# Optimization experiments

Measured on AMD Instinct MI355X. Metric: run time of the kernel, lower is better.

## Reference

```python
import jax, jax.numpy as jnp
import numpy as np

H = 1024          # hidden_size
NH = 16           # num_attention_heads
HD = H // NH      # head_dim = 64
FF = 4096         # intermediate_size
EPS = 1e-12       # layer_norm_eps
CLAMP = 1e9


def _layer_norm(x, gamma, beta):
    mu = jnp.mean(x, axis=-1, keepdims=True)
    var = jnp.mean(jnp.square(x - mu), axis=-1, keepdims=True)
    return (x - mu) * jax.lax.rsqrt(var + EPS) * gamma + beta


def setup_inputs() -> dict:
    key = jax.random.key(0)
    ks = jax.random.split(key, 12)
    B, S = 4, 2048
    s_h = 1.0 / np.sqrt(H)
    s_f = 1.0 / np.sqrt(FF)
    return {
        "hidden_states": jax.random.normal(ks[0], (B, S, H), jnp.float32),
        "Wq": jax.random.normal(ks[1], (H, H), jnp.float32) * s_h,
        "bq": jnp.zeros((H,), jnp.float32),
        "Wk": jax.random.normal(ks[2], (H, H), jnp.float32) * s_h,
        "bk": jnp.zeros((H,), jnp.float32),
        "Wv": jax.random.normal(ks[3], (H, H), jnp.float32) * s_h,
        "bv": jnp.zeros((H,), jnp.float32),
        "ln1_g": jnp.ones((H,), jnp.float32),
        "ln1_b": jnp.zeros((H,), jnp.float32),
        "W1": jax.random.normal(ks[4], (H, FF), jnp.float32) * s_h,
        "b1": jnp.zeros((FF,), jnp.float32),
        "W2": jax.random.normal(ks[5], (FF, H), jnp.float32) * s_f,
        "b2": jnp.zeros((H,), jnp.float32),
        "ln2_g": jnp.ones((H,), jnp.float32),
        "ln2_b": jnp.zeros((H,), jnp.float32),
    }


def reference(hidden_states, Wq, bq, Wk, bk, Wv, bv, ln1_g, ln1_b,
              W1, b1, W2, b2, ln2_g, ln2_b):
    B, S, _ = hidden_states.shape
    # QKV projections -> [B, NH, S, HD]
    def heads(x):
        return x.reshape(B, S, NH, HD).transpose(0, 2, 1, 3)
    q = heads(hidden_states @ Wq + bq)
    k = heads(hidden_states @ Wk + bk)
    v = heads(hidden_states @ Wv + bv)
    # manual attention: scale, clamp, softmax + 1e-9 epsilon
    scores = jnp.einsum('bhqd,bhkd->bhqk', q, k) / np.sqrt(HD)
    scores = jnp.clip(scores, -CLAMP, CLAMP)
    probs = jax.nn.softmax(scores, axis=-1) + 1e-9
    ctx = jnp.einsum('bhqk,bhkd->bhqd', probs, v)
    ctx = ctx.transpose(0, 2, 1, 3).reshape(B, S, NH * HD)
    # residual + LN (no output projection in this module)
    x = _layer_norm(hidden_states + ctx, ln1_g, ln1_b)
    # FFN with exact gelu + clamp
    inter = jax.nn.gelu(x @ W1 + b1, approximate=False)
    inter = jnp.clip(inter, -CLAMP, CLAMP)
    out = inter @ W2 + b2
    return _layer_norm(out + x, ln2_g, ln2_b)
```

## Files before the change

kernel.cpp:

```cpp
#include <hip/hip_runtime.h>
#include <math.h>


#define H_   1024
#define NH_  16
#define HD_  64
#define FF_  4096
#define S_   2048
#define B_   4
#define BS_  (B_ * S_)

#define EPI_NONE 0
#define EPI_GELU 1
#define EPI_QKV3 2

typedef unsigned short ushort_t;
typedef short v8s __attribute__((ext_vector_type(8)));
typedef float v4f __attribute__((ext_vector_type(4)));

__device__ __forceinline__ unsigned short f2bf(float f) {
    union { float f; unsigned int u; } v; v.f = f;
    unsigned int u = v.u;
    return (unsigned short)((u + 0x7fffu + ((u >> 16) & 1u)) >> 16);
}
__device__ __forceinline__ unsigned short f2bf_rn(float f) {
    union { float f; unsigned int u; } v; v.f = f;
    return (unsigned short)((v.u + 0x8000u) >> 16);
}
__device__ __forceinline__ float bf2f(unsigned short h) {
    union { unsigned int u; float f; } v; v.u = ((unsigned int)h) << 16;
    return v.f;
}

typedef __attribute__((address_space(1))) void gvoid;
typedef __attribute__((address_space(3))) void lvoid;
__device__ __forceinline__ void async16(const void* g, void* l) {
    __builtin_amdgcn_global_load_lds((gvoid*)g, (lvoid*)l, 16, 0, 0);
}

__global__ __launch_bounds__(256)
void cast_bf16_kernel(const float* __restrict__ x, ushort_t* __restrict__ y)
{
    const size_t i = ((size_t)blockIdx.x * 256 + threadIdx.x) * 4;
    float4 v = *(const float4*)&x[i];
    ushort4 o;
    o.x = f2bf(v.x); o.y = f2bf(v.y); o.z = f2bf(v.z); o.w = f2bf(v.w);
    *(ushort4*)&y[i] = o;
}

__global__ __launch_bounds__(256)
void cast_transpose_kernel(const float* __restrict__ W, ushort_t* __restrict__ Wt,
                           int K, int N)
{
    __shared__ float tile[32][33];
    const int tid = threadIdx.x;
    const int n0 = blockIdx.x * 32, k0 = blockIdx.y * 32;
    const int r  = tid >> 3;
    const int c4 = (tid & 7) * 4;
    float4 v = *(const float4*)&W[(size_t)(k0 + r) * N + n0 + c4];
    tile[r][c4 + 0] = v.x; tile[r][c4 + 1] = v.y;
    tile[r][c4 + 2] = v.z; tile[r][c4 + 3] = v.w;
    __syncthreads();
    ushort4 o;
    o.x = f2bf(tile[c4 + 0][r]); o.y = f2bf(tile[c4 + 1][r]);
    o.z = f2bf(tile[c4 + 2][r]); o.w = f2bf(tile[c4 + 3][r]);
    *(ushort4*)&Wt[(size_t)(n0 + r) * K + k0 + c4] = o;
}

__global__ __launch_bounds__(256)
void concat3_kernel(const float* __restrict__ a, const float* __restrict__ b,
                    const float* __restrict__ c, float* __restrict__ o)
{
    const int i = blockIdx.x * 256 + threadIdx.x;
    o[i] = (i < 1024) ? a[i] : (i < 2048) ? b[i - 1024] : c[i - 2048];
}

template <int EPI>
__global__ __launch_bounds__(256)
void bgemm_kernel(const ushort_t* __restrict__ A, const ushort_t* __restrict__ Bt,
                  const float* __restrict__ bias, void* __restrict__ Cout,
                  int M, int N, int K)
{
    __shared__ ushort_t Atile[128 * 32];
    __shared__ ushort_t Btile[128 * 32];

    const int tid  = threadIdx.x;
    const int wave = tid >> 6;
    const int lane = tid & 63;
    const int ml   = lane & 15;
    const int q8   = lane >> 4;
    const int wm   = wave >> 1, wn = wave & 1;
    const int blockM = blockIdx.y * 128;
    const int blockN = blockIdx.x * 128;

    v4f acc[4][4];
#pragma unroll
    for (int a = 0; a < 4; ++a)
#pragma unroll
        for (int b = 0; b < 4; ++b) acc[a][b] = (v4f)0.f;

    for (int kt = 0; kt < K; kt += 32) {
#pragma unroll
        for (int i = 0; i < 2; ++i) {
            const int chunk = (i * 4 + wave) * 64 + lane;
            const int row = chunk >> 2;
            const int kp  = chunk & 3;
            async16(A  + (size_t)(blockM + row) * K + kt + kp * 8, &Atile[chunk * 8]);
            async16(Bt + (size_t)(blockN + row) * K + kt + kp * 8, &Btile[chunk * 8]);
        }
        __syncthreads();

        v8s af[4], bfr[4];
#pragma unroll
        for (int a = 0; a < 4; ++a)
            af[a] = *(const v8s*)&Atile[(wm * 64 + a * 16 + ml) * 32 + q8 * 8];
#pragma unroll
        for (int b = 0; b < 4; ++b)
            bfr[b] = *(const v8s*)&Btile[(wn * 64 + b * 16 + ml) * 32 + q8 * 8];
#pragma unroll
        for (int a = 0; a < 4; ++a)
#pragma unroll
            for (int b = 0; b < 4; ++b)
                acc[a][b] = __builtin_amdgcn_mfma_f32_16x16x32_bf16(
                    af[a], bfr[b], acc[a][b], 0, 0, 0);
        __syncthreads();
    }

#pragma unroll
    for (int a = 0; a < 4; ++a) {
#pragma unroll
        for (int b = 0; b < 4; ++b) {
            const int n  = blockN + wn * 64 + b * 16 + ml;
            const float bn = bias[n];
            if (EPI == EPI_QKV3) {
                const int nn = n & 1023;
                const int hh = nn >> 6, dd = nn & 63;
                ushort_t* base = (ushort_t*)Cout + (size_t)(n >> 10) * ((size_t)BS_ * H_);
                if (n < 2048) {
#pragma unroll
                    for (int r = 0; r < 4; ++r) {
                        const int m = blockM + wm * 64 + a * 16 + q8 * 4 + r;
                        base[(((size_t)((m >> 11) * NH_ + hh)) * S_ + (m & 2047)) * HD_ + dd]
                            = f2bf(acc[a][b][r] + bn);
                    }
                } else {
                    const int m0 = blockM + wm * 64 + a * 16 + q8 * 4;
                    ushort4 pk;
                    pk.x = f2bf(acc[a][b][0] + bn);
                    pk.y = f2bf(acc[a][b][1] + bn);
                    pk.z = f2bf(acc[a][b][2] + bn);
                    pk.w = f2bf(acc[a][b][3] + bn);
                    *(ushort4*)&base[(((size_t)((m0 >> 11) * NH_ + hh)) * HD_ + dd) * S_
                                     + (m0 & 2047)] = pk;
                }
            } else {
#pragma unroll
                for (int r = 0; r < 4; ++r) {
                    const int m = blockM + wm * 64 + a * 16 + q8 * 4 + r;
                    float v = acc[a][b][r] + bn;
                    if (EPI == EPI_GELU) {
                        v = v * 0.5f * (1.f + erff(v * 0.70710678118654752f));
                        v = fminf(fmaxf(v, -1e9f), 1e9f);
                        ((ushort_t*)Cout)[(size_t)m * N + n] = f2bf(v);
                    } else {
                        ((float*)Cout)[(size_t)m * N + n] = v;
                    }
                }
            }
        }
    }
}

__global__ __launch_bounds__(256)
void vsum_kernel(const ushort_t* __restrict__ VT, float* __restrict__ vsum)
{
    const int bh   = blockIdx.x;
    const int tid  = threadIdx.x;
    const int d    = tid >> 2;
    const int part = tid & 3;
    const ushort_t* p = VT + (size_t)bh * HD_ * S_ + (size_t)d * S_ + part * 512;
    float acc = 0.f;
    for (int i = 0; i < 512; i += 4) {
        ushort4 u = *(const ushort4*)&p[i];
        acc += (bf2f(u.x) + bf2f(u.y)) + (bf2f(u.z) + bf2f(u.w));
    }
    acc += __shfl_xor(acc, 1);
    acc += __shfl_xor(acc, 2);
    if (part == 0) vsum[bh * HD_ + d] = acc;
}

__global__ __launch_bounds__(256)
void flash_kernel(const ushort_t* __restrict__ Q, const ushort_t* __restrict__ Kg,
                  const ushort_t* __restrict__ VT, const float* __restrict__ vsum,
                  float* __restrict__ ctx)
{
    __shared__ ushort_t Qs[64 * 64];
    __shared__ ushort_t Ks[64 * 64];
    __shared__ ushort_t Vs[64 * 64];
    __shared__ ushort_t Pt[64 * 72];

    const int bh   = blockIdx.y;
    const int q0   = blockIdx.x * 64;
    const int tid  = threadIdx.x;
    const int wave = tid >> 6;
    const int lane = tid & 63;
    const int ml   = lane & 15;
    const int q8   = lane >> 4;
    const int sw   = ml & 7;

    const ushort_t* Qp = Q  + (size_t)bh * S_ * HD_ + (size_t)q0 * HD_;
    const ushort_t* Kp = Kg + (size_t)bh * S_ * HD_;
    const ushort_t* Vp = VT + (size_t)bh * HD_ * S_;

#pragma unroll
    for (int i = 0; i < 2; ++i) {
        const int chunk = i * 256 + tid;
        const int row = chunk >> 3, c = chunk & 7;
        async16(Qp + (size_t)row * HD_ + ((c ^ (row & 7)) * 8), &Qs[chunk * 8]);
    }

    const float C_ = 0.18033688011112042f;
    float l_r = 0.f;
    v4f o[4];
#pragma unroll
    for (int g = 0; g < 4; ++g) o[g] = (v4f)0.f;
    v8s qf0, qf1;

    const int prow = (wave * 16 + ml) * 72;

    for (int t = 0; t < S_ / 64; ++t) {
        const int kv0 = t * 64;
        __syncthreads();
#pragma unroll
        for (int i = 0; i < 2; ++i) {
            const int chunk = i * 256 + tid;
            const int row = chunk >> 3, c = chunk & 7;
            async16(Kp + (size_t)(kv0 + row) * HD_ + ((c ^ (row & 7)) * 8),
                    &Ks[chunk * 8]);
        }
#pragma unroll
        for (int i = 0; i < 2; ++i) {
            const int chunk = i * 256 + tid;
            const int row = chunk >> 3, c = chunk & 7;
            async16(Vp + (size_t)row * S_ + kv0 + ((c ^ (row & 7)) * 8),
                    &Vs[chunk * 8]);
        }
        __syncthreads();

        if (t == 0) {
            const int qrow = wave * 16 + ml;
            qf0 = *(const v8s*)&Qs[qrow * 64 + ((q8 ^ sw) * 8)];
            qf1 = *(const v8s*)&Qs[qrow * 64 + (((q8 + 4) ^ sw) * 8)];
        }

#pragma unroll
        for (int a = 0; a < 4; ++a) {
            const int krow = (a * 16 + ml) * 64;
            v8s kf0 = *(const v8s*)&Ks[krow + ((q8 ^ sw) * 8)];
            v8s kf1 = *(const v8s*)&Ks[krow + (((q8 + 4) ^ sw) * 8)];
            v4f z = (v4f)0.f;
            z = __builtin_amdgcn_mfma_f32_16x16x32_bf16(kf0, qf0, z, 0, 0, 0);
            z = __builtin_amdgcn_mfma_f32_16x16x32_bf16(kf1, qf1, z, 0, 0, 0);
            const float p0 = __builtin_exp2f(z[0] * C_);
            const float p1 = __builtin_exp2f(z[1] * C_);
            const float p2 = __builtin_exp2f(z[2] * C_);
            const float p3 = __builtin_exp2f(z[3] * C_);
            l_r += (p0 + p1) + (p2 + p3);
            ushort4 pk;
            pk.x = f2bf_rn(p0); pk.y = f2bf_rn(p1);
            pk.z = f2bf_rn(p2); pk.w = f2bf_rn(p3);
            *(ushort4*)&Pt[prow + a * 16 + q8 * 4] = pk;
        }

        v8s pf0 = *(const v8s*)&Pt[prow + q8 * 8];
        v8s pf1 = *(const v8s*)&Pt[prow + 32 + q8 * 8];
#pragma unroll
        for (int g = 0; g < 4; ++g) {
            const int vrow = (g * 16 + ml) * 64;
            v8s vf0 = *(const v8s*)&Vs[vrow + ((q8 ^ sw) * 8)];
            v8s vf1 = *(const v8s*)&Vs[vrow + (((q8 + 4) ^ sw) * 8)];
            o[g] = __builtin_amdgcn_mfma_f32_16x16x32_bf16(vf0, pf0, o[g], 0, 0, 0);
            o[g] = __builtin_amdgcn_mfma_f32_16x16x32_bf16(vf1, pf1, o[g], 0, 0, 0);
        }
    }

    l_r += __shfl_xor(l_r, 16);
    l_r += __shfl_xor(l_r, 32);

    const int bb = bh >> 4, hh = bh & 15;
    const float linv = 1.f / l_r;
    const int srow = q0 + wave * 16 + ml;
    float* cp = ctx + ((size_t)(bb * S_ + srow)) * H_ + hh * HD_;
#pragma unroll
    for (int g = 0; g < 4; ++g) {
        float4 vs4 = *(const float4*)&vsum[bh * HD_ + g * 16 + q8 * 4];
        float4 ov;
        ov.x = o[g][0] * linv + 1e-9f * vs4.x;
        ov.y = o[g][1] * linv + 1e-9f * vs4.y;
        ov.z = o[g][2] * linv + 1e-9f * vs4.z;
        ov.w = o[g][3] * linv + 1e-9f * vs4.w;
        *(float4*)&cp[g * 16 + q8 * 4] = ov;
    }
}

template <bool WB>
__global__ __launch_bounds__(256)
void add_ln_kernel(const float* __restrict__ A, const float* __restrict__ Bv,
                   const float* __restrict__ gamma, const float* __restrict__ beta,
                   float* __restrict__ out, ushort_t* __restrict__ outb)
{
    const int row = blockIdx.x;
    const int tid = threadIdx.x;
    const float* a = A  + (size_t)row * H_;
    const float* b = Bv + (size_t)row * H_;

    float4 av = *(const float4*)&a[tid * 4];
    float4 bv = *(const float4*)&b[tid * 4];
    float x[4] = { av.x + bv.x, av.y + bv.y, av.z + bv.z, av.w + bv.w };

    float s  = x[0] + x[1] + x[2] + x[3];
    float s2 = x[0]*x[0] + x[1]*x[1] + x[2]*x[2] + x[3]*x[3];
#pragma unroll
    for (int off = 1; off < 64; off <<= 1) {
        s  += __shfl_xor(s,  off);
        s2 += __shfl_xor(s2, off);
    }
    __shared__ float rs[8];
    const int wave = tid >> 6, lane = tid & 63;
    if (lane == 0) { rs[wave] = s; rs[4 + wave] = s2; }
    __syncthreads();
    const float sum  = rs[0] + rs[1] + rs[2] + rs[3];
    const float sum2 = rs[4] + rs[5] + rs[6] + rs[7];
    const float mu   = sum * (1.f / H_);
    const float var  = sum2 * (1.f / H_) - mu * mu;
    const float rstd = rsqrtf(var + 1e-12f);

    float4 gv = *(const float4*)&gamma[tid * 4];
    float4 be = *(const float4*)&beta[tid * 4];
    float4 ov;
    ov.x = (x[0] - mu) * rstd * gv.x + be.x;
    ov.y = (x[1] - mu) * rstd * gv.y + be.y;
    ov.z = (x[2] - mu) * rstd * gv.z + be.z;
    ov.w = (x[3] - mu) * rstd * gv.w + be.w;
    *(float4*)&out[(size_t)row * H_ + tid * 4] = ov;
    if (WB) {
        ushort4 ob;
        ob.x = f2bf(ov.x); ob.y = f2bf(ov.y); ob.z = f2bf(ov.z); ob.w = f2bf(ov.w);
        *(ushort4*)&outb[(size_t)row * H_ + tid * 4] = ob;
    }
}

extern "C" void kernel_launch(void* const* d_in, const int* in_sizes, int n_in,
                              void* d_out, int out_size, void* d_ws, size_t ws_size,
                              hipStream_t stream)
{
    const float* hidden = (const float*)d_in[0];
    const float* Wq     = (const float*)d_in[1];
    const float* bq     = (const float*)d_in[2];
    const float* Wk     = (const float*)d_in[3];
    const float* bk     = (const float*)d_in[4];
    const float* Wv     = (const float*)d_in[5];
    const float* bv     = (const float*)d_in[6];
    const float* ln1_g  = (const float*)d_in[7];
    const float* ln1_b  = (const float*)d_in[8];
    const float* W1     = (const float*)d_in[9];
    const float* b1     = (const float*)d_in[10];
    const float* W2     = (const float*)d_in[11];
    const float* b2     = (const float*)d_in[12];
    const float* ln2_g  = (const float*)d_in[13];
    const float* ln2_b  = (const float*)d_in[14];

    char* ws = (char*)d_ws;
    const size_t MB = 1024 * 1024;
    ushort_t* Xb    = (ushort_t*)(ws + 0);
    ushort_t* x1b   = (ushort_t*)(ws + 0);
    ushort_t* Wqt   = (ushort_t*)(ws + 16 * MB);
    ushort_t* Wkt   = (ushort_t*)(ws + 18 * MB);
    ushort_t* Wvt   = (ushort_t*)(ws + 20 * MB);
    ushort_t* W1t   = (ushort_t*)(ws + 16 * MB);
    ushort_t* W2t   = (ushort_t*)(ws + 24 * MB);
    ushort_t* q     = (ushort_t*)(ws + 32 * MB);
    ushort_t* k     = (ushort_t*)(ws + 48 * MB);
    ushort_t* vt    = (ushort_t*)(ws + 64 * MB);
    float*    ctx   = (float*)(ws + 80 * MB);
    ushort_t* inter = (ushort_t*)(ws + 32 * MB);
    float*    bcat  = (float*)(ws + 96 * MB);
    float*    vsum  = (float*)(ws + 96 * MB + 16384);
    float*    out2  = (float*)(ws + 96 * MB);
    float*    x1    = (float*)(ws + 128 * MB);
    float*    out   = (float*)d_out;

    const dim3 blk(256);

    cast_bf16_kernel<<<dim3(BS_ * H_ / 1024), blk, 0, stream>>>(hidden, Xb);
    cast_transpose_kernel<<<dim3(32, 32),  blk, 0, stream>>>(Wq, Wqt, H_, H_);
    cast_transpose_kernel<<<dim3(32, 32),  blk, 0, stream>>>(Wk, Wkt, H_, H_);
    cast_transpose_kernel<<<dim3(32, 32),  blk, 0, stream>>>(Wv, Wvt, H_, H_);
    cast_transpose_kernel<<<dim3(32, 128), blk, 0, stream>>>(W2, W2t, FF_, H_);
    concat3_kernel<<<dim3(12), blk, 0, stream>>>(bq, bk, bv, bcat);

    bgemm_kernel<EPI_QKV3><<<dim3(24, 64), blk, 0, stream>>>(
        Xb, Wqt, bcat, q, BS_, 3 * H_, H_);

    cast_transpose_kernel<<<dim3(128, 32), blk, 0, stream>>>(W1, W1t, H_, FF_);

    vsum_kernel<<<dim3(B_ * NH_), blk, 0, stream>>>(vt, vsum);

    flash_kernel<<<dim3(S_ / 64, B_ * NH_), blk, 0, stream>>>(q, k, vt, vsum, ctx);

    add_ln_kernel<true><<<dim3(BS_), blk, 0, stream>>>(hidden, ctx, ln1_g, ln1_b, x1, x1b);

    bgemm_kernel<EPI_GELU><<<dim3(32, 64), blk, 0, stream>>>(x1b, W1t, b1, inter, BS_, FF_, H_);

    bgemm_kernel<EPI_NONE><<<dim3(8, 64), blk, 0, stream>>>(inter, W2t, b2, out2, BS_, H_, FF_);

    add_ln_kernel<false><<<dim3(BS_), blk, 0, stream>>>(out2, x1, ln2_g, ln2_b, out, nullptr);
}
```

Measured before the change: 619.4 us.

## Double flash query tile per block and stage QK epilogue through LDS

The flash attention kernel now handles 128 query rows per block (32 per wave, as two 16-row groups). Each loaded K/V tile is therefore reused across twice as many queries, halving K/V global and LDS traffic per query, at the cost of more registers. The Q staging buffer is reused as the P buffer, and P packing uses a byte-permute helper. The QKV GEMM epilogue for Q and K now writes through a padded LDS tile so each head row goes out as contiguous 16-byte stores instead of scattered 2-byte writes, which requires a larger shared buffer in all GEMM instantiations.

```diff
diff --git a/kernel.cpp b/kernel.cpp
--- a/kernel.cpp
+++ b/kernel.cpp
@@ -17,19 +17,20 @@
 typedef unsigned short ushort_t;
 typedef short v8s __attribute__((ext_vector_type(8)));
 typedef float v4f __attribute__((ext_vector_type(4)));
+typedef unsigned int v2u __attribute__((ext_vector_type(2)));
 
 __device__ __forceinline__ unsigned short f2bf(float f) {
     union { float f; unsigned int u; } v; v.f = f;
     unsigned int u = v.u;
     return (unsigned short)((u + 0x7fffu + ((u >> 16) & 1u)) >> 16);
 }
-__device__ __forceinline__ unsigned short f2bf_rn(float f) {
-    union { float f; unsigned int u; } v; v.f = f;
-    return (unsigned short)((v.u + 0x8000u) >> 16);
-}
 __device__ __forceinline__ float bf2f(unsigned short h) {
     union { unsigned int u; float f; } v; v.u = ((unsigned int)h) << 16;
     return v.f;
+}
+__device__ __forceinline__ unsigned int pk2bf(float a, float b) {
+    union { float f; unsigned int u; } ua, ub; ua.f = a; ub.f = b;
+    return __builtin_amdgcn_perm(ub.u + 0x8000u, ua.u + 0x8000u, 0x07060302u);
 }
 
 typedef __attribute__((address_space(1))) void gvoid;
@@ -81,8 +82,9 @@
                   const float* __restrict__ bias, void* __restrict__ Cout,
                   int M, int N, int K)
 {
-    __shared__ ushort_t Atile[128 * 32];
-    __shared__ ushort_t Btile[128 * 32];
+    __shared__ ushort_t smem[17408];
+    ushort_t* Atile = smem;
+    ushort_t* Btile = smem + 4096;
 
     const int tid  = threadIdx.x;
     const int wave = tid >> 6;
@@ -126,6 +128,31 @@
         __syncthreads();
     }
 
+    if (EPI == EPI_QKV3 && blockN < 2048) {
+#pragma unroll
+        for (int a = 0; a < 4; ++a)
+#pragma unroll
+            for (int b = 0; b < 4; ++b) {
+                const int n_loc = wn * 64 + b * 16 + ml;
+                const float bn = bias[blockN + n_loc];
+#pragma unroll
+                for (int r = 0; r < 4; ++r)
+                    smem[(wm * 64 + a * 16 + q8 * 4 + r) * 136 + n_loc] =
+                        f2bf(acc[a][b][r] + bn);
+            }
+        __syncthreads();
+        const int row  = tid >> 1, half = tid & 1;
+        const int m    = blockM + row;
+        const int hh   = ((blockN & 1023) >> 6) + half;
+        ushort_t* gp = (ushort_t*)Cout + (blockN >= 1024 ? (size_t)BS_ * H_ : 0)
+                     + (((size_t)((m >> 11) * NH_ + hh)) * S_ + (m & 2047)) * HD_;
+        const ushort_t* lp = &smem[row * 136 + half * 64];
+#pragma unroll
+        for (int j = 0; j < 8; ++j)
+            *(uint4*)&gp[j * 8] = *(const uint4*)&lp[j * 8];
+        return;
+    }
+
 #pragma unroll
     for (int a = 0; a < 4; ++a) {
 #pragma unroll
@@ -135,24 +162,15 @@
             if (EPI == EPI_QKV3) {
                 const int nn = n & 1023;
                 const int hh = nn >> 6, dd = nn & 63;
-                ushort_t* base = (ushort_t*)Cout + (size_t)(n >> 10) * ((size_t)BS_ * H_);
-                if (n < 2048) {
-#pragma unroll
-                    for (int r = 0; r < 4; ++r) {
-                        const int m = blockM + wm * 64 + a * 16 + q8 * 4 + r;
-                        base[(((size_t)((m >> 11) * NH_ + hh)) * S_ + (m & 2047)) * HD_ + dd]
-                            = f2bf(acc[a][b][r] + bn);
-                    }
-                } else {
-                    const int m0 = blockM + wm * 64 + a * 16 + q8 * 4;
-                    ushort4 pk;
-                    pk.x = f2bf(acc[a][b][0] + bn);
-                    pk.y = f2bf(acc[a][b][1] + bn);
-                    pk.z = f2bf(acc[a][b][2] + bn);
-                    pk.w = f2bf(acc[a][b][3] + bn);
-                    *(ushort4*)&base[(((size_t)((m0 >> 11) * NH_ + hh)) * HD_ + dd) * S_
-                                     + (m0 & 2047)] = pk;
-                }
+                ushort_t* base = (ushort_t*)Cout + (size_t)2 * BS_ * H_;
+                const int m0 = blockM + wm * 64 + a * 16 + q8 * 4;
+                ushort4 pk;
+                pk.x = f2bf(acc[a][b][0] + bn);
+                pk.y = f2bf(acc[a][b][1] + bn);
+                pk.z = f2bf(acc[a][b][2] + bn);
+                pk.w = f2bf(acc[a][b][3] + bn);
+                *(ushort4*)&base[(((size_t)((m0 >> 11) * NH_ + hh)) * HD_ + dd) * S_
+                                 + (m0 & 2047)] = pk;
             } else {
 #pragma unroll
                 for (int r = 0; r < 4; ++r) {
@@ -189,18 +207,17 @@
     if (part == 0) vsum[bh * HD_ + d] = acc;
 }
 
-__global__ __launch_bounds__(256)
+__global__ __launch_bounds__(256, 4)
 void flash_kernel(const ushort_t* __restrict__ Q, const ushort_t* __restrict__ Kg,
                   const ushort_t* __restrict__ VT, const float* __restrict__ vsum,
                   float* __restrict__ ctx)
 {
-    __shared__ ushort_t Qs[64 * 64];
+    __shared__ ushort_t PtQ[128 * 72];
     __shared__ ushort_t Ks[64 * 64];
     __shared__ ushort_t Vs[64 * 64];
-    __shared__ ushort_t Pt[64 * 72];
 
     const int bh   = blockIdx.y;
-    const int q0   = blockIdx.x * 64;
+    const int q0   = blockIdx.x * 128;
     const int tid  = threadIdx.x;
     const int wave = tid >> 6;
     const int lane = tid & 63;
@@ -213,20 +230,28 @@
     const ushort_t* Vp = VT + (size_t)bh * HD_ * S_;
 
 #pragma unroll
-    for (int i = 0; i < 2; ++i) {
+    for (int i = 0; i < 4; ++i) {
         const int chunk = i * 256 + tid;
         const int row = chunk >> 3, c = chunk & 7;
-        async16(Qp + (size_t)row * HD_ + ((c ^ (row & 7)) * 8), &Qs[chunk * 8]);
+        async16(Qp + (size_t)row * HD_ + ((c ^ (row & 7)) * 8), &PtQ[chunk * 8]);
+    }
+    __syncthreads();
+
+    v8s qf[2][2];
+#pragma unroll
+    for (int qg = 0; qg < 2; ++qg) {
+        const int qrow = wave * 32 + qg * 16 + ml;
+        qf[qg][0] = *(const v8s*)&PtQ[qrow * 64 + ((q8 ^ sw) * 8)];
+        qf[qg][1] = *(const v8s*)&PtQ[qrow * 64 + (((q8 + 4) ^ sw) * 8)];
     }
 
     const float C_ = 0.18033688011112042f;
-    float l_r = 0.f;
-    v4f o[4];
-#pragma unroll
-    for (int g = 0; g < 4; ++g) o[g] = (v4f)0.f;
-    v8s qf0, qf1;
-
-    const int prow = (wave * 16 + ml) * 72;
+    float l_r[2] = {0.f, 0.f};
+    v4f o[2][4];
+#pragma unroll
+    for (int qg = 0; qg < 2; ++qg)
+#pragma unroll
+        for (int g = 0; g < 4; ++g) o[qg][g] = (v4f)0.f;
 
     for (int t = 0; t < S_ / 64; ++t) {
         const int kv0 = t * 64;
@@ -247,59 +272,69 @@
         }
         __syncthreads();
 
-        if (t == 0) {
-            const int qrow = wave * 16 + ml;
-            qf0 = *(const v8s*)&Qs[qrow * 64 + ((q8 ^ sw) * 8)];
-            qf1 = *(const v8s*)&Qs[qrow * 64 + (((q8 + 4) ^ sw) * 8)];
-        }
-
 #pragma unroll
         for (int a = 0; a < 4; ++a) {
             const int krow = (a * 16 + ml) * 64;
             v8s kf0 = *(const v8s*)&Ks[krow + ((q8 ^ sw) * 8)];
             v8s kf1 = *(const v8s*)&Ks[krow + (((q8 + 4) ^ sw) * 8)];
-            v4f z = (v4f)0.f;
-            z = __builtin_amdgcn_mfma_f32_16x16x32_bf16(kf0, qf0, z, 0, 0, 0);
-            z = __builtin_amdgcn_mfma_f32_16x16x32_bf16(kf1, qf1, z, 0, 0, 0);
-            const float p0 = __builtin_exp2f(z[0] * C_);
-            const float p1 = __builtin_exp2f(z[1] * C_);
-            const float p2 = __builtin_exp2f(z[2] * C_);
-            const float p3 = __builtin_exp2f(z[3] * C_);
-            l_r += (p0 + p1) + (p2 + p3);
-            ushort4 pk;
-            pk.x = f2bf_rn(p0); pk.y = f2bf_rn(p1);
-            pk.z = f2bf_rn(p2); pk.w = f2bf_rn(p3);
-            *(ushort4*)&Pt[prow + a * 16 + q8 * 4] = pk;
-        }
-
-        v8s pf0 = *(const v8s*)&Pt[prow + q8 * 8];
-        v8s pf1 = *(const v8s*)&Pt[prow + 32 + q8 * 8];
+#pragma unroll
+            for (int qg = 0; qg < 2; ++qg) {
+                v4f z = (v4f)0.f;
+                z = __builtin_amdgcn_mfma_f32_16x16x32_bf16(kf0, qf[qg][0], z, 0, 0, 0);
+                z = __builtin_amdgcn_mfma_f32_16x16x32_bf16(kf1, qf[qg][1], z, 0, 0, 0);
+                const float p0 = __builtin_exp2f(z[0] * C_);
+                const float p1 = __builtin_exp2f(z[1] * C_);
+                const float p2 = __builtin_exp2f(z[2] * C_);
+                const float p3 = __builtin_exp2f(z[3] * C_);
+                l_r[qg] += (p0 + p1) + (p2 + p3);
+                v2u pk;
+                pk.x = pk2bf(p0, p1);
+                pk.y = pk2bf(p2, p3);
+                *(v2u*)&PtQ[(wave * 32 + qg * 16 + ml) * 72 + a * 16 + q8 * 4] = pk;
+            }
+        }
+
+        v8s pf[2][2];
+#pragma unroll
+        for (int qg = 0; qg < 2; ++qg) {
+            const int prow = (wave * 32 + qg * 16 + ml) * 72;
+            pf[qg][0] = *(const v8s*)&PtQ[prow + q8 * 8];
+            pf[qg][1] = *(const v8s*)&PtQ[prow + 32 + q8 * 8];
+        }
 #pragma unroll
         for (int g = 0; g < 4; ++g) {
             const int vrow = (g * 16 + ml) * 64;
             v8s vf0 = *(const v8s*)&Vs[vrow + ((q8 ^ sw) * 8)];
             v8s vf1 = *(const v8s*)&Vs[vrow + (((q8 + 4) ^ sw) * 8)];
-            o[g] = __builtin_amdgcn_mfma_f32_16x16x32_bf16(vf0, pf0, o[g], 0, 0, 0);
-            o[g] = __builtin_amdgcn_mfma_f32_16x16x32_bf16(vf1, pf1, o[g], 0, 0, 0);
-        }
-    }
-
-    l_r += __shfl_xor(l_r, 16);
-    l_r += __shfl_xor(l_r, 32);
+#pragma unroll
+            for (int qg = 0; qg < 2; ++qg) {
+                o[qg][g] = __builtin_amdgcn_mfma_f32_16x16x32_bf16(vf0, pf[qg][0],
+                                                                   o[qg][g], 0, 0, 0);
+                o[qg][g] = __builtin_amdgcn_mfma_f32_16x16x32_bf16(vf1, pf[qg][1],
+                                                                   o[qg][g], 0, 0, 0);
+            }
+        }
+    }
 
     const int bb = bh >> 4, hh = bh & 15;
-    const float linv = 1.f / l_r;
-    const int srow = q0 + wave * 16 + ml;
-    float* cp = ctx + ((size_t)(bb * S_ + srow)) * H_ + hh * HD_;
-#pragma unroll
-    for (int g = 0; g < 4; ++g) {
-        float4 vs4 = *(const float4*)&vsum[bh * HD_ + g * 16 + q8 * 4];
-        float4 ov;
-        ov.x = o[g][0] * linv + 1e-9f * vs4.x;
-        ov.y = o[g][1] * linv + 1e-9f * vs4.y;
-        ov.z = o[g][2] * linv + 1e-9f * vs4.z;
-        ov.w = o[g][3] * linv + 1e-9f * vs4.w;
-        *(float4*)&cp[g * 16 + q8 * 4] = ov;
+#pragma unroll
+    for (int qg = 0; qg < 2; ++qg) {
+        float l = l_r[qg];
+        l += __shfl_xor(l, 16);
+        l += __shfl_xor(l, 32);
+        const float linv = 1.f / l;
+        const int srow = q0 + wave * 32 + qg * 16 + ml;
+        float* cp = ctx + ((size_t)(bb * S_ + srow)) * H_ + hh * HD_;
+#pragma unroll
+        for (int g = 0; g < 4; ++g) {
+            float4 vs4 = *(const float4*)&vsum[bh * HD_ + g * 16 + q8 * 4];
+            float4 ov;
+            ov.x = o[qg][g][0] * linv + 1e-9f * vs4.x;
+            ov.y = o[qg][g][1] * linv + 1e-9f * vs4.y;
+            ov.z = o[qg][g][2] * linv + 1e-9f * vs4.z;
+            ov.w = o[qg][g][3] * linv + 1e-9f * vs4.w;
+            *(float4*)&cp[g * 16 + q8 * 4] = ov;
+        }
     }
 }
 
@@ -406,7 +441,7 @@
 
     vsum_kernel<<<dim3(B_ * NH_), blk, 0, stream>>>(vt, vsum);
 
-    flash_kernel<<<dim3(S_ / 64, B_ * NH_), blk, 0, stream>>>(q, k, vt, vsum, ctx);
+    flash_kernel<<<dim3(S_ / 128, B_ * NH_), blk, 0, stream>>>(q, k, vt, vsum, ctx);
 
     add_ln_kernel<true><<<dim3(BS_), blk, 0, stream>>>(hidden, ctx, ln1_g, ln1_b, x1, x1b);
 
```

Measured after the change: 626.9 us. About the same (+1.2%).
